# Kernel tuning notes

Measured on AMD Instinct MI355X. Metric: run time of the kernel, lower is better.

The kernel has to match this reference:

```python
import jax, jax.numpy as jnp
import numpy as np

N, K = 150000, 27
C1, C2 = 64, 64
CLAMP = 1.0


def _lrelu(v):
    return jnp.where(v >= 0, v, 0.2 * v)


def _sparse_conv(feats, nbr_idx, W):
    # feats: [N, Cin], nbr_idx: [N, K], W: [K, Cin, Cout]
    # gather-GEMM-scatter sparse conv; scan over the 27 fixed kernel offsets
    acc0 = jnp.zeros((feats.shape[0], W.shape[-1]), feats.dtype)

    def step(acc, kw):
        idx, Wk = kw  # idx: [N], Wk: [Cin, Cout]
        return acc + feats[idx] @ Wk, None

    acc, _ = jax.lax.scan(step, acc0, (nbr_idx.T, W))
    return acc


def _bottleneck(x, nbr_idx, w1, w2, w3):
    h = _lrelu(_sparse_conv(x, nbr_idx, w1))  # kxkxk conv
    h = _lrelu(h @ w2)                        # 1x1x1 conv
    return _sparse_conv(h, nbr_idx, w3)       # kxkxk conv


def setup_inputs() -> dict:
    key = jax.random.key(0)
    ks = jax.random.split(key, 14)
    x = jax.random.normal(ks[0], (N, C1 + C2), jnp.float32)
    nbr_idx = jax.random.randint(ks[1], (N, K), 0, N, jnp.int32)
    s = 0.1  # xavier-like small scale
    d = {"x": x, "nbr_idx": nbr_idx}
    names = ["g1", "g2", "h1", "h2"]
    for i, nm in enumerate(names):
        d[nm + "_w1"] = jax.random.normal(ks[2 + 3 * i], (K, C2 if nm in ("g2", "h2") else C1, C1 if nm in ("g2", "h2") else C2), jnp.float32) * s
        co = C1 if nm in ("g2", "h2") else C2
        d[nm + "_w2"] = jax.random.normal(ks[3 + 3 * i], (co, co), jnp.float32) * s
        d[nm + "_w3"] = jax.random.normal(ks[4 + 3 * i], (K, co, co), jnp.float32) * s
    return d


def reference(x, nbr_idx, g1_w1, g1_w2, g1_w3, g2_w1, g2_w2, g2_w3,
              h1_w1, h1_w2, h1_w3, h2_w1, h2_w2, h2_w3):
    x1 = x[:, :C1]
    x2 = x[:, C1:C1 + C2]
    # forward (reverse=False) affine coupling
    s1 = jnp.exp(CLAMP * (jax.nn.sigmoid(_bottleneck(x2, nbr_idx, g2_w1, g2_w2, g2_w3)) * 2 - 1))
    y1 = x1 * s1 + _bottleneck(x2, nbr_idx, h2_w1, h2_w2, h2_w3)
    s2 = jnp.exp(CLAMP * (jax.nn.sigmoid(_bottleneck(y1, nbr_idx, g1_w1, g1_w2, g1_w3)) * 2 - 1))
    y2 = x2 * s2 + _bottleneck(y1, nbr_idx, h1_w1, h1_w2, h1_w3)
    return jnp.concatenate([y1, y2], axis=1)
```

## Files before the change

kernel.cpp:

```cpp
#include <hip/hip_runtime.h>
#include <stdint.h>

typedef unsigned short u16;
typedef __bf16 bf16x8 __attribute__((ext_vector_type(8)));
typedef float f32x4 __attribute__((ext_vector_type(4)));

#define NNODES 150000
#define KNBR 27
#define LDX 128
#define MR 128
#define APAD 72
#define WSU 8192

#define WAITVM(N) asm volatile("s_waitcnt vmcnt(" #N ")" ::: "memory")

static __device__ __forceinline__ void gl_lds16(const u16* g, u16* l){
  __builtin_amdgcn_global_load_lds((const __attribute__((address_space(1))) void*)g,
                                   (__attribute__((address_space(3))) void*)l, 16, 0, 0);
}

static __device__ __forceinline__ u16 f2bf(float f){
  union { float f; uint32_t i; } v; v.f = f;
  uint32_t x = v.i;
  uint32_t r = (x + 0x7fffu + ((x >> 16) & 1u)) >> 16;
  return (u16)r;
}
static __device__ __forceinline__ float lrelu(float v){ return v >= 0.f ? v : 0.2f*v; }

__global__ void reformat_w(const float* __restrict__ src, u16* __restrict__ dst, int ksteps){
  int idx = blockIdx.x*256 + threadIdx.x;
  int total = ksteps*4*64;
  if (idx >= total) return;
  int lane = idx & 63;
  int ctile = (idx >> 6) & 3;
  int t = idx >> 8;
  int quad = lane >> 4, m = lane & 15;
  union { u16 h[8]; float4 v; } tmp;
  const float* s = src + ((size_t)(t*32 + quad*8))*64 + ctile*16 + m;
  #pragma unroll
  for (int j=0;j<8;j++) tmp.h[j] = f2bf(s[j*64]);
  *reinterpret_cast<float4*>(dst + (size_t)idx*8) = tmp.v;
}

__global__ void conv_x2(const float* __restrict__ x, u16* __restrict__ sb){
  int idx = blockIdx.x*256 + threadIdx.x;
  int e = idx*8;
  if (e >= NNODES*64) return;
  int row = e >> 6, col = e & 63;
  const float* s = x + (size_t)row*LDX + 64 + col;
  float4 a = *reinterpret_cast<const float4*>(s);
  float4 b = *reinterpret_cast<const float4*>(s+4);
  union { u16 h[8]; float4 v; } t;
  t.h[0]=f2bf(a.x); t.h[1]=f2bf(a.y); t.h[2]=f2bf(a.z); t.h[3]=f2bf(a.w);
  t.h[4]=f2bf(b.x); t.h[5]=f2bf(b.y); t.h[6]=f2bf(b.z); t.h[7]=f2bf(b.w);
  *reinterpret_cast<float4*>(sb + e) = t.v;
}

#define STAGE_W(s, wG, wH) { \
  u16* db_ = ws + ((s)&1)*WSU; \
  _Pragma("unroll") \
  for (int j_=0;j_<2;j_++){ \
    int c_ = wv*2 + j_; \
    int mat_ = (c_>>2)&1; int tt_ = c_>>3; int ct_ = c_&3; \
    const u16* src_ = (mat_ ? (wH) : (wG)) + ((size_t)(2*(s)+tt_))*2048 + (size_t)ct_*512 + (size_t)lane*8; \
    gl_lds16(src_, db_ + (size_t)c_*512); \
  } }

__global__ __launch_bounds__(512,4) void conv1_fused(
    const u16* __restrict__ sb,
    const int* __restrict__ nbr,
    const u16* __restrict__ wb1g, const u16* __restrict__ wb1h,
    const u16* __restrict__ wb2g, const u16* __restrict__ wb2h,
    u16* __restrict__ u)
{
  extern __shared__ char smem[];
  u16* ws    = (u16*)smem;
  int* s_idx = (int*)(smem + 2*WSU*2);
  u16* sa    = (u16*)smem;
  u16* w2l   = (u16*)(smem + 36864);

  int tid = threadIdx.x;
  int row0 = blockIdx.x * MR;
  for (int i = tid; i < MR*KNBR; i += 512){
    int r = i / KNBR, kk = i - r*KNBR;
    int row = row0 + r;
    s_idx[i] = (row < NNODES) ? nbr[row*KNBR + kk] : 0;
  }
  __syncthreads();

  int lane = tid & 63;
  int wv = tid >> 6;
  int quad = lane >> 4, m = lane & 15;
  int qoff = quad * 8;
  const int* idx = &s_idx[(wv*16 + m)*KNBR];

  f32x4 acc[2][4];
  f32x4 zz = {0.f,0.f,0.f,0.f};
  #pragma unroll
  for (int mt2=0;mt2<2;mt2++)
    #pragma unroll
    for (int i=0;i<4;i++) acc[mt2][i] = zz;

  bf16x8 as[3][2];

  #define LOAD_A1(s, d0, d1) { \
    const u16* r_ = sb + (size_t)idx[s]*64 + qoff; \
    d0 = *reinterpret_cast<const bf16x8*>(r_); \
    d1 = *reinterpret_cast<const bf16x8*>(r_ + 32); }

  STAGE_W(0, wb1g, wb1h); __builtin_amdgcn_sched_barrier(0);
  LOAD_A1(0, as[0][0], as[0][1]); __builtin_amdgcn_sched_barrier(0);
  LOAD_A1(1, as[1][0], as[1][1]); __builtin_amdgcn_sched_barrier(0);
  LOAD_A1(2, as[2][0], as[2][1]);

  #pragma unroll
  for (int k=0;k<KNBR;k++){
    if (k == 0)       { WAITVM(4); }
    else if (k <= 24) { WAITVM(2); }
    else              { WAITVM(0); }
    __builtin_amdgcn_s_barrier();

    if (k+1 < KNBR) { STAGE_W(k+1, wb1g, wb1h); }
    __builtin_amdgcn_sched_barrier(0);

    const u16* wsb = ws + (k&1)*WSU;
    #pragma unroll
    for (int tt=0;tt<2;tt++){
      bf16x8 af = as[k%3][tt];
      #pragma unroll
      for (int mt2=0;mt2<2;mt2++){
        #pragma unroll
        for (int ct=0;ct<4;ct++){
          bf16x8 b = *reinterpret_cast<const bf16x8*>(wsb + ((tt*2+mt2)*4+ct)*512 + (size_t)lane*8);
          acc[mt2][ct] = __builtin_amdgcn_mfma_f32_16x16x32_bf16(af, b, acc[mt2][ct], 0,0,0);
        }
      }
    }
    if (k+3 < KNBR) { LOAD_A1(k+3, as[k%3][0], as[k%3][1]); }
  }
  __syncthreads();

  #pragma unroll
  for (int j_=0;j_<2;j_++){
    int cc = wv*2 + j_;
    int mt2_ = cc>>3;
    const u16* src_ = (mt2_ ? wb2h : wb2g) + (size_t)(cc&7)*512 + (size_t)lane*8;
    gl_lds16(src_, w2l + (size_t)cc*512);
  }

  #pragma unroll
  for (int mt2=0;mt2<2;mt2++){
    #pragma unroll
    for (int ct=0;ct<4;ct++){
      #pragma unroll
      for (int i=0;i<4;i++){
        int rl = wv*16 + quad*4 + i;
        sa[mt2*MR*APAD + rl*APAD + ct*16 + m] = f2bf(lrelu(acc[mt2][ct][i]));
      }
    }
  }
  WAITVM(0);
  __syncthreads();

  f32x4 d[2][4];
  #pragma unroll
  for (int mt2=0;mt2<2;mt2++)
    #pragma unroll
    for (int i=0;i<4;i++) d[mt2][i] = zz;
  #pragma unroll
  for (int c=0;c<2;c++){
    #pragma unroll
    for (int mt2=0;mt2<2;mt2++){
      bf16x8 a = *reinterpret_cast<const bf16x8*>(&sa[mt2*MR*APAD + (wv*16 + m)*APAD + c*32 + qoff]);
      #pragma unroll
      for (int ct=0;ct<4;ct++){
        bf16x8 b = *reinterpret_cast<const bf16x8*>(w2l + (size_t)(mt2*8 + c*4 + ct)*512 + (size_t)lane*8);
        d[mt2][ct] = __builtin_amdgcn_mfma_f32_16x16x32_bf16(a, b, d[mt2][ct], 0,0,0);
      }
    }
  }
  #pragma unroll
  for (int mt2=0;mt2<2;mt2++){
    #pragma unroll
    for (int ct=0;ct<4;ct++){
      #pragma unroll
      for (int i=0;i<4;i++){
        int row = row0 + wv*16 + quad*4 + i;
        if (row < NNODES){
          u[(size_t)row*128 + mt2*64 + ct*16 + m] = f2bf(lrelu(d[mt2][ct][i]));
        }
      }
    }
  }
  #undef LOAD_A1
}

__global__ __launch_bounds__(512,4) void conv2_coupling(
    const u16* __restrict__ ub,
    const int* __restrict__ nbr,
    const u16* __restrict__ wbg, const u16* __restrict__ wbh,
    const float* __restrict__ x, int xcol0,
    float* __restrict__ out, int ycol0,
    u16* __restrict__ yb, int write_yb)
{
  extern __shared__ char smem[];
  u16* ws    = (u16*)smem;
  int* s_idx = (int*)(smem + 2*WSU*2);

  int tid = threadIdx.x;
  int row0 = blockIdx.x * MR;
  for (int i = tid; i < MR*KNBR; i += 512){
    int r = i / KNBR, kk = i - r*KNBR;
    int row = row0 + r;
    s_idx[i] = (row < NNODES) ? nbr[row*KNBR + kk] : 0;
  }
  __syncthreads();

  int lane = tid & 63;
  int wv = tid >> 6;
  int quad = lane >> 4, m = lane & 15;
  int qoff = quad * 8;
  const int* idx = &s_idx[(wv*16 + m)*KNBR];

  f32x4 accg[4], acch[4];
  f32x4 zz = {0.f,0.f,0.f,0.f};
  #pragma unroll
  for (int i=0;i<4;i++){ accg[i]=zz; acch[i]=zz; }

  bf16x8 as[2][4];

  #define LOAD_A2(s, d0, d1, d2, d3) { \
    const u16* r_ = ub + (size_t)idx[s]*128 + qoff; \
    d0 = *reinterpret_cast<const bf16x8*>(r_); \
    d1 = *reinterpret_cast<const bf16x8*>(r_ + 32); \
    d2 = *reinterpret_cast<const bf16x8*>(r_ + 64); \
    d3 = *reinterpret_cast<const bf16x8*>(r_ + 96); }

  STAGE_W(0, wbg, wbh); __builtin_amdgcn_sched_barrier(0);
  LOAD_A2(0, as[0][0], as[0][1], as[0][2], as[0][3]); __builtin_amdgcn_sched_barrier(0);
  LOAD_A2(1, as[1][0], as[1][1], as[1][2], as[1][3]);

  #pragma unroll
  for (int k=0;k<KNBR;k++){
    if (k < 26) { WAITVM(4); }
    else        { WAITVM(0); }
    __builtin_amdgcn_s_barrier();

    if (k+1 < KNBR) { STAGE_W(k+1, wbg, wbh); }
    __builtin_amdgcn_sched_barrier(0);

    const u16* wsb = ws + (k&1)*WSU;
    #pragma unroll
    for (int tt=0;tt<2;tt++){
      bf16x8 ag = as[k&1][tt];
      bf16x8 ah = as[k&1][2+tt];
      #pragma unroll
      for (int ct=0;ct<4;ct++){
        bf16x8 bg = *reinterpret_cast<const bf16x8*>(wsb + ((tt*2+0)*4+ct)*512 + (size_t)lane*8);
        accg[ct] = __builtin_amdgcn_mfma_f32_16x16x32_bf16(ag, bg, accg[ct], 0,0,0);
      }
      #pragma unroll
      for (int ct=0;ct<4;ct++){
        bf16x8 bh = *reinterpret_cast<const bf16x8*>(wsb + ((tt*2+1)*4+ct)*512 + (size_t)lane*8);
        acch[ct] = __builtin_amdgcn_mfma_f32_16x16x32_bf16(ah, bh, acch[ct], 0,0,0);
      }
    }
    if (k+2 < KNBR) { LOAD_A2(k+2, as[k&1][0], as[k&1][1], as[k&1][2], as[k&1][3]); }
  }

  #pragma unroll
  for (int ct=0;ct<4;ct++){
    #pragma unroll
    for (int i=0;i<4;i++){
      int row = row0 + wv*16 + quad*4 + i;
      if (row < NNODES){
        int col = ct*16 + m;
        float bg = accg[ct][i];
        float bh = acch[ct][i];
        float s = 1.f/(1.f + __expf(-bg));
        s = __expf(2.f*s - 1.f);
        float xv = x[(size_t)row*LDX + xcol0 + col];
        float y = xv*s + bh;
        out[(size_t)row*LDX + ycol0 + col] = y;
        if (write_yb) yb[(size_t)row*64 + col] = f2bf(y);
      }
    }
  }
  #undef LOAD_A2
}

extern "C" void kernel_launch(void* const* d_in, const int* in_sizes, int n_in,
                              void* d_out, int out_size, void* d_ws, size_t ws_size,
                              hipStream_t stream)
{
  const float* x   = (const float*)d_in[0];
  const int*   nbr = (const int*)d_in[1];
  const float* g1_w1=(const float*)d_in[2],  *g1_w2=(const float*)d_in[3],  *g1_w3=(const float*)d_in[4];
  const float* g2_w1=(const float*)d_in[5],  *g2_w2=(const float*)d_in[6],  *g2_w3=(const float*)d_in[7];
  const float* h1_w1=(const float*)d_in[8],  *h1_w2=(const float*)d_in[9],  *h1_w3=(const float*)d_in[10];
  const float* h2_w1=(const float*)d_in[11], *h2_w2=(const float*)d_in[12], *h2_w3=(const float*)d_in[13];
  float* out = (float*)d_out;
  u16* ws = (u16*)d_ws;

  const size_t WBB = (size_t)54*4*64*8;
  const size_t WBS = (size_t)2*4*64*8;
  u16* p = ws;
  u16* wb_g2_1=p; p+=WBB;  u16* wb_h2_1=p; p+=WBB;
  u16* wb_g2_2=p; p+=WBS;  u16* wb_h2_2=p; p+=WBS;
  u16* wb_g2_3=p; p+=WBB;  u16* wb_h2_3=p; p+=WBB;
  u16* wb_g1_1=p; p+=WBB;  u16* wb_h1_1=p; p+=WBB;
  u16* wb_g1_2=p; p+=WBS;  u16* wb_h1_2=p; p+=WBS;
  u16* wb_g1_3=p; p+=WBB;  u16* wb_h1_3=p; p+=WBB;
  u16* ub = p; p += (size_t)NNODES*128;
  u16* sb = p; p += (size_t)NNODES*64;

  reformat_w<<<54,256,0,stream>>>(g2_w1, wb_g2_1, 54);
  reformat_w<<<54,256,0,stream>>>(h2_w1, wb_h2_1, 54);
  reformat_w<<<2,256,0,stream>>>(g2_w2, wb_g2_2, 2);
  reformat_w<<<2,256,0,stream>>>(h2_w2, wb_h2_2, 2);
  reformat_w<<<54,256,0,stream>>>(g2_w3, wb_g2_3, 54);
  reformat_w<<<54,256,0,stream>>>(h2_w3, wb_h2_3, 54);
  reformat_w<<<54,256,0,stream>>>(g1_w1, wb_g1_1, 54);
  reformat_w<<<54,256,0,stream>>>(h1_w1, wb_h1_1, 54);
  reformat_w<<<2,256,0,stream>>>(g1_w2, wb_g1_2, 2);
  reformat_w<<<2,256,0,stream>>>(h1_w2, wb_h1_2, 2);
  reformat_w<<<54,256,0,stream>>>(g1_w3, wb_g1_3, 54);
  reformat_w<<<54,256,0,stream>>>(h1_w3, wb_h1_3, 54);

  conv_x2<<<(NNODES*64/8 + 255)/256, 256, 0, stream>>>(x, sb);

  int nblk = (NNODES + MR - 1)/MR;
  size_t c1_lds = 53248;
  size_t c2_lds = (size_t)2*WSU*2 + (size_t)MR*KNBR*4;

  conv1_fused<<<nblk,512,c1_lds,stream>>>(sb, nbr, wb_g2_1, wb_h2_1, wb_g2_2, wb_h2_2, ub);
  conv2_coupling<<<nblk,512,c2_lds,stream>>>(ub, nbr, wb_g2_3, wb_h2_3, x, 0, out, 0, sb, 1);
  conv1_fused<<<nblk,512,c1_lds,stream>>>(sb, nbr, wb_g1_1, wb_h1_1, wb_g1_2, wb_h1_2, ub);
  conv2_coupling<<<nblk,512,c2_lds,stream>>>(ub, nbr, wb_g1_3, wb_h1_3, x, 64, out, 64, sb, 0);
}
```

Baseline: 745.6 us.

## Process two kernel offsets per barrier window and keep neighbor indices in registers

```diff
diff --git a/kernel.cpp b/kernel.cpp
--- a/kernel.cpp
+++ b/kernel.cpp
@@ -4,13 +4,16 @@
 typedef unsigned short u16;
 typedef __bf16 bf16x8 __attribute__((ext_vector_type(8)));
 typedef float f32x4 __attribute__((ext_vector_type(4)));
+typedef int i32x4u __attribute__((ext_vector_type(4), aligned(4)));
+typedef int i32x2u __attribute__((ext_vector_type(2), aligned(4)));
 
 #define NNODES 150000
 #define KNBR 27
 #define LDX 128
 #define MR 128
 #define APAD 72
-#define WSU 8192
+#define WSU2 16384
+#define NWIN 14
 
 #define WAITVM(N) asm volatile("s_waitcnt vmcnt(" #N ")" ::: "memory")
 
@@ -56,14 +59,36 @@
   *reinterpret_cast<float4*>(sb + e) = t.v;
 }
 
-#define STAGE_W(s, wG, wH) { \
-  u16* db_ = ws + ((s)&1)*WSU; \
+#define LOAD_NID(nbrp, rsel) { \
+  const int* nr_ = (nbrp) + (size_t)(rsel)*KNBR; \
   _Pragma("unroll") \
-  for (int j_=0;j_<2;j_++){ \
-    int c_ = wv*2 + j_; \
-    int mat_ = (c_>>2)&1; int tt_ = c_>>3; int ct_ = c_&3; \
-    const u16* src_ = (mat_ ? (wH) : (wG)) + ((size_t)(2*(s)+tt_))*2048 + (size_t)ct_*512 + (size_t)lane*8; \
-    gl_lds16(src_, db_ + (size_t)c_*512); \
+  for (int j_=0;j_<6;j_++){ \
+    i32x4u v_ = *reinterpret_cast<const i32x4u*>(nr_ + 4*j_); \
+    nid[4*j_+0]=v_[0]; nid[4*j_+1]=v_[1]; nid[4*j_+2]=v_[2]; nid[4*j_+3]=v_[3]; \
+  } \
+  { i32x2u v_ = *reinterpret_cast<const i32x2u*>(nr_ + 24); \
+    nid[24]=v_[0]; nid[25]=v_[1]; } \
+  nid[26] = nr_[26]; }
+
+#define STAGE_WIN(w_, wG, wH) { \
+  u16* db_ = ws + ((w_)&1)*WSU2; \
+  if (2*(w_)+1 < KNBR){ \
+    _Pragma("unroll") \
+    for (int j_=0;j_<4;j_++){ \
+      int c_ = wv*4 + j_; \
+      int ks_ = c_>>4, cc_ = c_&15; \
+      int mat_=(cc_>>2)&1, tt_=cc_>>3, ct_=cc_&3; \
+      const u16* src_ = (mat_? (wH):(wG)) + ((size_t)(2*(2*(w_)+ks_)+tt_))*2048 + (size_t)ct_*512 + (size_t)lane*8; \
+      gl_lds16(src_, db_ + (size_t)c_*512); \
+    } \
+  } else { \
+    _Pragma("unroll") \
+    for (int j_=0;j_<2;j_++){ \
+      int c_ = wv*2 + j_; \
+      int mat_=(c_>>2)&1, tt_=c_>>3, ct_=c_&3; \
+      const u16* src_ = (mat_? (wH):(wG)) + ((size_t)(2*(2*(w_))+tt_))*2048 + (size_t)ct_*512 + (size_t)lane*8; \
+      gl_lds16(src_, db_ + (size_t)c_*512); \
+    } \
   } }
 
 __global__ __launch_bounds__(512,4) void conv1_fused(
@@ -74,25 +99,21 @@
     u16* __restrict__ u)
 {
   extern __shared__ char smem[];
-  u16* ws    = (u16*)smem;
-  int* s_idx = (int*)(smem + 2*WSU*2);
-  u16* sa    = (u16*)smem;
-  u16* w2l   = (u16*)(smem + 36864);
+  u16* ws  = (u16*)smem;
+  u16* sa  = (u16*)smem;
+  u16* w2l = (u16*)(smem + 36864);
 
   int tid = threadIdx.x;
-  int row0 = blockIdx.x * MR;
-  for (int i = tid; i < MR*KNBR; i += 512){
-    int r = i / KNBR, kk = i - r*KNBR;
-    int row = row0 + r;
-    s_idx[i] = (row < NNODES) ? nbr[row*KNBR + kk] : 0;
-  }
-  __syncthreads();
-
   int lane = tid & 63;
   int wv = tid >> 6;
   int quad = lane >> 4, m = lane & 15;
   int qoff = quad * 8;
-  const int* idx = &s_idx[(wv*16 + m)*KNBR];
+  int row0 = blockIdx.x * MR;
+  int myrow = row0 + wv*16 + m;
+  int rsel = (myrow < NNODES) ? myrow : 0;
+
+  int nid[KNBR];
+  LOAD_NID(nbr, rsel);
 
   f32x4 acc[2][4];
   f32x4 zz = {0.f,0.f,0.f,0.f};
@@ -101,42 +122,50 @@
     #pragma unroll
     for (int i=0;i<4;i++) acc[mt2][i] = zz;
 
-  bf16x8 as[3][2];
-
-  #define LOAD_A1(s, d0, d1) { \
-    const u16* r_ = sb + (size_t)idx[s]*64 + qoff; \
-    d0 = *reinterpret_cast<const bf16x8*>(r_); \
-    d1 = *reinterpret_cast<const bf16x8*>(r_ + 32); }
-
-  STAGE_W(0, wb1g, wb1h); __builtin_amdgcn_sched_barrier(0);
-  LOAD_A1(0, as[0][0], as[0][1]); __builtin_amdgcn_sched_barrier(0);
-  LOAD_A1(1, as[1][0], as[1][1]); __builtin_amdgcn_sched_barrier(0);
-  LOAD_A1(2, as[2][0], as[2][1]);
-
-  #pragma unroll
-  for (int k=0;k<KNBR;k++){
-    if (k == 0)       { WAITVM(4); }
-    else if (k <= 24) { WAITVM(2); }
+  bf16x8 as1[2][2][2];
+
+  #define LOADW1(w_) { \
+    { const u16* r_ = sb + (size_t)nid[2*(w_)]*64 + qoff; \
+      as1[(w_)&1][0][0] = *reinterpret_cast<const bf16x8*>(r_); \
+      as1[(w_)&1][0][1] = *reinterpret_cast<const bf16x8*>(r_ + 32); } \
+    if (2*(w_)+1 < KNBR){ \
+      const u16* r_ = sb + (size_t)nid[2*(w_)+1]*64 + qoff; \
+      as1[(w_)&1][1][0] = *reinterpret_cast<const bf16x8*>(r_); \
+      as1[(w_)&1][1][1] = *reinterpret_cast<const bf16x8*>(r_ + 32); } }
+
+  STAGE_WIN(0, wb1g, wb1h); __builtin_amdgcn_sched_barrier(0);
+  LOADW1(0); __builtin_amdgcn_sched_barrier(0);
+  LOADW1(1);
+
+  #pragma unroll
+  for (int w=0; w<NWIN; ++w){
+    if (w < 12)       { WAITVM(4); }
+    else if (w == 12) { WAITVM(2); }
     else              { WAITVM(0); }
     __builtin_amdgcn_s_barrier();
 
-    if (k+1 < KNBR) { STAGE_W(k+1, wb1g, wb1h); }
+    if (w+1 < NWIN) { STAGE_WIN(w+1, wb1g, wb1h); }
     __builtin_amdgcn_sched_barrier(0);
 
-    const u16* wsb = ws + (k&1)*WSU;
-    #pragma unroll
-    for (int tt=0;tt<2;tt++){
-      bf16x8 af = as[k%3][tt];
-      #pragma unroll
-      for (int mt2=0;mt2<2;mt2++){
+    #pragma unroll
+    for (int ks=0; ks<2; ks++){
+      if (2*w + ks < KNBR){
+        const u16* wsb = ws + (w&1)*WSU2 + ks*8192;
         #pragma unroll
-        for (int ct=0;ct<4;ct++){
-          bf16x8 b = *reinterpret_cast<const bf16x8*>(wsb + ((tt*2+mt2)*4+ct)*512 + (size_t)lane*8);
-          acc[mt2][ct] = __builtin_amdgcn_mfma_f32_16x16x32_bf16(af, b, acc[mt2][ct], 0,0,0);
+        for (int tt=0;tt<2;tt++){
+          bf16x8 af = as1[w&1][ks][tt];
+          #pragma unroll
+          for (int mt2=0;mt2<2;mt2++){
+            #pragma unroll
+            for (int ct=0;ct<4;ct++){
+              bf16x8 b = *reinterpret_cast<const bf16x8*>(wsb + ((tt*2+mt2)*4+ct)*512 + (size_t)lane*8);
+              acc[mt2][ct] = __builtin_amdgcn_mfma_f32_16x16x32_bf16(af, b, acc[mt2][ct], 0,0,0);
+            }
+          }
         }
       }
     }
-    if (k+3 < KNBR) { LOAD_A1(k+3, as[k%3][0], as[k%3][1]); }
+    if (w+2 < NWIN) { LOADW1(w+2); }
   }
   __syncthreads();
 
@@ -192,7 +221,7 @@
       }
     }
   }
-  #undef LOAD_A1
+  #undef LOADW1
 }
 
 __global__ __launch_bounds__(512,4) void conv2_coupling(
@@ -204,68 +233,76 @@
     u16* __restrict__ yb, int write_yb)
 {
   extern __shared__ char smem[];
-  u16* ws    = (u16*)smem;
-  int* s_idx = (int*)(smem + 2*WSU*2);
+  u16* ws = (u16*)smem;
 
   int tid = threadIdx.x;
-  int row0 = blockIdx.x * MR;
-  for (int i = tid; i < MR*KNBR; i += 512){
-    int r = i / KNBR, kk = i - r*KNBR;
-    int row = row0 + r;
-    s_idx[i] = (row < NNODES) ? nbr[row*KNBR + kk] : 0;
-  }
-  __syncthreads();
-
   int lane = tid & 63;
   int wv = tid >> 6;
   int quad = lane >> 4, m = lane & 15;
   int qoff = quad * 8;
-  const int* idx = &s_idx[(wv*16 + m)*KNBR];
+  int row0 = blockIdx.x * MR;
+  int myrow = row0 + wv*16 + m;
+  int rsel = (myrow < NNODES) ? myrow : 0;
+
+  int nid[KNBR];
+  LOAD_NID(nbr, rsel);
 
   f32x4 accg[4], acch[4];
   f32x4 zz = {0.f,0.f,0.f,0.f};
   #pragma unroll
   for (int i=0;i<4;i++){ accg[i]=zz; acch[i]=zz; }
 
-  bf16x8 as[2][4];
-
-  #define LOAD_A2(s, d0, d1, d2, d3) { \
-    const u16* r_ = ub + (size_t)idx[s]*128 + qoff; \
-    d0 = *reinterpret_cast<const bf16x8*>(r_); \
-    d1 = *reinterpret_cast<const bf16x8*>(r_ + 32); \
-    d2 = *reinterpret_cast<const bf16x8*>(r_ + 64); \
-    d3 = *reinterpret_cast<const bf16x8*>(r_ + 96); }
-
-  STAGE_W(0, wbg, wbh); __builtin_amdgcn_sched_barrier(0);
-  LOAD_A2(0, as[0][0], as[0][1], as[0][2], as[0][3]); __builtin_amdgcn_sched_barrier(0);
-  LOAD_A2(1, as[1][0], as[1][1], as[1][2], as[1][3]);
-
-  #pragma unroll
-  for (int k=0;k<KNBR;k++){
-    if (k < 26) { WAITVM(4); }
-    else        { WAITVM(0); }
+  bf16x8 as2[2][2][4];
+
+  #define LOADW2(w_) { \
+    { const u16* r_ = ub + (size_t)nid[2*(w_)]*128 + qoff; \
+      as2[(w_)&1][0][0] = *reinterpret_cast<const bf16x8*>(r_); \
+      as2[(w_)&1][0][1] = *reinterpret_cast<const bf16x8*>(r_ + 32); \
+      as2[(w_)&1][0][2] = *reinterpret_cast<const bf16x8*>(r_ + 64); \
+      as2[(w_)&1][0][3] = *reinterpret_cast<const bf16x8*>(r_ + 96); } \
+    if (2*(w_)+1 < KNBR){ \
+      const u16* r_ = ub + (size_t)nid[2*(w_)+1]*128 + qoff; \
+      as2[(w_)&1][1][0] = *reinterpret_cast<const bf16x8*>(r_); \
+      as2[(w_)&1][1][1] = *reinterpret_cast<const bf16x8*>(r_ + 32); \
+      as2[(w_)&1][1][2] = *reinterpret_cast<const bf16x8*>(r_ + 64); \
+      as2[(w_)&1][1][3] = *reinterpret_cast<const bf16x8*>(r_ + 96); } }
+
+  STAGE_WIN(0, wbg, wbh); __builtin_amdgcn_sched_barrier(0);
+  LOADW2(0); __builtin_amdgcn_sched_barrier(0);
+  LOADW2(1);
+
+  #pragma unroll
+  for (int w=0; w<NWIN; ++w){
+    if (w < 12)       { WAITVM(8); }
+    else if (w == 12) { WAITVM(4); }
+    else              { WAITVM(0); }
     __builtin_amdgcn_s_barrier();
 
-    if (k+1 < KNBR) { STAGE_W(k+1, wbg, wbh); }
+    if (w+1 < NWIN) { STAGE_WIN(w+1, wbg, wbh); }
     __builtin_amdgcn_sched_barrier(0);
 
-    const u16* wsb = ws + (k&1)*WSU;
-    #pragma unroll
-    for (int tt=0;tt<2;tt++){
-      bf16x8 ag = as[k&1][tt];
-      bf16x8 ah = as[k&1][2+tt];
-      #pragma unroll
-      for (int ct=0;ct<4;ct++){
-        bf16x8 bg = *reinterpret_cast<const bf16x8*>(wsb + ((tt*2+0)*4+ct)*512 + (size_t)lane*8);
-        accg[ct] = __builtin_amdgcn_mfma_f32_16x16x32_bf16(ag, bg, accg[ct], 0,0,0);
-      }
-      #pragma unroll
-      for (int ct=0;ct<4;ct++){
-        bf16x8 bh = *reinterpret_cast<const bf16x8*>(wsb + ((tt*2+1)*4+ct)*512 + (size_t)lane*8);
-        acch[ct] = __builtin_amdgcn_mfma_f32_16x16x32_bf16(ah, bh, acch[ct], 0,0,0);
-      }
-    }
-    if (k+2 < KNBR) { LOAD_A2(k+2, as[k&1][0], as[k&1][1], as[k&1][2], as[k&1][3]); }
+    #pragma unroll
+    for (int ks=0; ks<2; ks++){
+      if (2*w + ks < KNBR){
+        const u16* wsb = ws + (w&1)*WSU2 + ks*8192;
+        #pragma unroll
+        for (int tt=0;tt<2;tt++){
+          bf16x8 ag = as2[w&1][ks][tt];
+          bf16x8 ah = as2[w&1][ks][2+tt];
+          #pragma unroll
+          for (int ct=0;ct<4;ct++){
+            bf16x8 bg = *reinterpret_cast<const bf16x8*>(wsb + ((tt*2+0)*4+ct)*512 + (size_t)lane*8);
+            accg[ct] = __builtin_amdgcn_mfma_f32_16x16x32_bf16(ag, bg, accg[ct], 0,0,0);
+          }
+          #pragma unroll
+          for (int ct=0;ct<4;ct++){
+            bf16x8 bh = *reinterpret_cast<const bf16x8*>(wsb + ((tt*2+1)*4+ct)*512 + (size_t)lane*8);
+            acch[ct] = __builtin_amdgcn_mfma_f32_16x16x32_bf16(ah, bh, acch[ct], 0,0,0);
+          }
+        }
+      }
+    }
+    if (w+2 < NWIN) { LOADW2(w+2); }
   }
 
   #pragma unroll
@@ -286,7 +323,7 @@
       }
     }
   }
-  #undef LOAD_A2
+  #undef LOADW2
 }
 
 extern "C" void kernel_launch(void* const* d_in, const int* in_sizes, int n_in,
@@ -330,11 +367,10 @@
   conv_x2<<<(NNODES*64/8 + 255)/256, 256, 0, stream>>>(x, sb);
 
   int nblk = (NNODES + MR - 1)/MR;
-  size_t c1_lds = 53248;
-  size_t c2_lds = (size_t)2*WSU*2 + (size_t)MR*KNBR*4;
-
-  conv1_fused<<<nblk,512,c1_lds,stream>>>(sb, nbr, wb_g2_1, wb_h2_1, wb_g2_2, wb_h2_2, ub);
-  conv2_coupling<<<nblk,512,c2_lds,stream>>>(ub, nbr, wb_g2_3, wb_h2_3, x, 0, out, 0, sb, 1);
-  conv1_fused<<<nblk,512,c1_lds,stream>>>(sb, nbr, wb_g1_1, wb_h1_1, wb_g1_2, wb_h1_2, ub);
-  conv2_coupling<<<nblk,512,c2_lds,stream>>>(ub, nbr, wb_g1_3, wb_h1_3, x, 64, out, 64, sb, 0);
-}
+  size_t lds_sz = (size_t)2*WSU2*2;
+
+  conv1_fused<<<nblk,512,lds_sz,stream>>>(sb, nbr, wb_g2_1, wb_h2_1, wb_g2_2, wb_h2_2, ub);
+  conv2_coupling<<<nblk,512,lds_sz,stream>>>(ub, nbr, wb_g2_3, wb_h2_3, x, 0, out, 0, sb, 1);
+  conv1_fused<<<nblk,512,lds_sz,stream>>>(sb, nbr, wb_g1_1, wb_h1_1, wb_g1_2, wb_h1_2, ub);
+  conv2_coupling<<<nblk,512,lds_sz,stream>>>(ub, nbr, wb_g1_3, wb_h1_3, x, 64, out, 64, sb, 0);
+}
```

Result: slower. 792.4 us (+6.3%).
